# Performance work log

Hardware: AMD Instinct MI355X
Metric: run time of the kernel (lower is better)

The kernel has to match this reference:

```python
import jax, jax.numpy as jnp
import numpy as np

N = 8192
D = 256
DENSITY = 0.02  # ~164 neighbors per node


def setup_inputs() -> dict:
    key = jax.random.key(0)
    k1, k2, k3, k4 = jax.random.split(key, 4)
    inputs = jax.random.normal(k1, (N, D), dtype=jnp.float32)
    vals = jax.random.uniform(k2, (N, N), dtype=jnp.float32, minval=0.1, maxval=1.0)
    mask = jax.random.uniform(k3, (N, N), dtype=jnp.float32) < DENSITY
    adj = jnp.where(mask, vals, 0.0)
    H_v = 0.1 * jax.random.normal(k4, (D, 1), dtype=jnp.float32)
    return {"inputs": inputs, "adj": adj, "H_v": H_v}


def reference(inputs, adj, H_v):
    # scores[j] = inputs[j] . H_v  -> sparse values v_ij = adj_ij * scores[j]
    scores = jnp.squeeze(inputs @ H_v, -1)            # [N]
    mask = adj != 0.0                                  # nonzero pattern of SparseTensor
    logits = adj * scores[None, :]                     # [N, N]
    neg = jnp.asarray(jnp.finfo(logits.dtype).min, logits.dtype)
    logits = jnp.where(mask, logits, neg)
    # sparse softmax: normalize only over nonzero entries per row
    m = jnp.max(logits, axis=1, keepdims=True)
    e = jnp.where(mask, jnp.exp(logits - m), 0.0)
    s = jnp.sum(e, axis=1, keepdims=True)
    weights = e / jnp.where(s > 0, s, 1.0)             # empty rows -> all-zero weights
    # sparse_tensor_dense_matmul(weights, inputs)
    return weights @ inputs                            # [N, D]
```

## Files before the change

### kernel.cpp

```cpp
#include <hip/hip_runtime.h>

#define NN 8192
#define DD 256
#define CAP 1024

typedef float v4f __attribute__((ext_vector_type(4)));
typedef unsigned short u16x4 __attribute__((ext_vector_type(4)));

__device__ __forceinline__ unsigned short f2bf_rne(float x) {
    unsigned u = __float_as_uint(x);
    u += 0x7fffu + ((u >> 16) & 1u);
    return (unsigned short)(u >> 16);
}

__device__ __forceinline__ float4 bf4_to_f4(u16x4 u) {
    float4 r;
    r.x = __uint_as_float((unsigned)u.x << 16);
    r.y = __uint_as_float((unsigned)u.y << 16);
    r.z = __uint_as_float((unsigned)u.z << 16);
    r.w = __uint_as_float((unsigned)u.w << 16);
    return r;
}

__global__ __launch_bounds__(256) void prep_kernel(const float* __restrict__ inputs,
                                                   const float* __restrict__ Hv,
                                                   float* __restrict__ scores,
                                                   unsigned short* __restrict__ ib) {
    int wave = threadIdx.x >> 6;
    int lane = threadIdx.x & 63;
    int row  = blockIdx.x * 4 + wave;
    float4 v = ((const float4*)(inputs + (size_t)row * DD))[lane];
    u16x4 u;
    u.x = f2bf_rne(v.x); u.y = f2bf_rne(v.y); u.z = f2bf_rne(v.z); u.w = f2bf_rne(v.w);
    ((u16x4*)(ib + (size_t)row * DD))[lane] = u;
    float4 h = ((const float4*)Hv)[lane];
    float s = v.x * h.x + v.y * h.y + v.z * h.z + v.w * h.w;
    #pragma unroll
    for (int off = 32; off > 0; off >>= 1) s += __shfl_down(s, off, 64);
    if (lane == 0) scores[row] = s;
}

template <bool BF16>
__device__ __forceinline__ float4 load_row4(const float* __restrict__ inputs,
                                            const unsigned short* __restrict__ ib,
                                            int j, int lane4) {
    if (BF16) return bf4_to_f4(*(const u16x4*)(ib + (size_t)j * DD + lane4));
    else      return *(const float4*)(inputs + (size_t)j * DD + lane4);
}

template <bool BF16>
__device__ __forceinline__ void gather_accum(const float2* __restrict__ s_je,
                                             int kbeg, int kend,
                                             const float* __restrict__ inputs,
                                             const unsigned short* __restrict__ ib,
                                             int lane, int lane4,
                                             float4& acc, float& ssum) {
    for (int base = kbeg; base < kend; base += 64) {
        int nb = kend - base; nb = nb > 64 ? 64 : nb;
        float2 je = s_je[base + (lane < nb ? lane : 0)];
        int jl = __float_as_int(je.x);
        int el = __float_as_int(je.y);
        int m = 0;
        for (; m + 8 <= nb; m += 8) {
            int js[8]; float es[8]; float4 f[8];
            #pragma unroll
            for (int u = 0; u < 8; ++u) {
                js[u] = __builtin_amdgcn_readlane(jl, m + u);
                es[u] = __uint_as_float(__builtin_amdgcn_readlane(el, m + u));
            }
            #pragma unroll
            for (int u = 0; u < 8; ++u) f[u] = load_row4<BF16>(inputs, ib, js[u], lane4);
            #pragma unroll
            for (int u = 0; u < 8; ++u) {
                acc.x += es[u] * f[u].x; acc.y += es[u] * f[u].y;
                acc.z += es[u] * f[u].z; acc.w += es[u] * f[u].w;
                ssum  += es[u];
            }
        }
        for (; m < nb; ++m) {
            int   j = __builtin_amdgcn_readlane(jl, m);
            float e = __uint_as_float(__builtin_amdgcn_readlane(el, m));
            float4 f = load_row4<BF16>(inputs, ib, j, lane4);
            acc.x += e * f.x; acc.y += e * f.y; acc.z += e * f.z; acc.w += e * f.w;
            ssum += e;
        }
    }
}

template <bool BF16>
__global__ __launch_bounds__(256) void attn_kernel(const float* __restrict__ adj,
                                                   const float* __restrict__ inputs,
                                                   const unsigned short* __restrict__ ib,
                                                   const float* __restrict__ scores,
                                                   float* __restrict__ out) {
    __shared__ float2 s_je[CAP];
    __shared__ int   s_wsum[4];
    __shared__ float s_ssum[4];
    __shared__ int   s_cnt;
    __shared__ float s_red[4 * DD];

    const int row   = blockIdx.x;
    const int tid   = threadIdx.x;
    const int lane  = tid & 63;
    const int wave  = tid >> 6;
    const int lane4 = lane * 4;

    const v4f* arow4 = (const v4f*)(adj + (size_t)row * NN);
    v4f a[8];
#pragma unroll
    for (int c = 0; c < 8; ++c) a[c] = __builtin_nontemporal_load(&arow4[c * 256 + tid]);

    int nz = 0;
#pragma unroll
    for (int c = 0; c < 8; ++c)
        nz += (a[c].x != 0.f) + (a[c].y != 0.f) + (a[c].z != 0.f) + (a[c].w != 0.f);

    int pre = nz;
#pragma unroll
    for (int off = 1; off < 64; off <<= 1) {
        int t = __shfl_up(pre, off, 64);
        if (lane >= off) pre += t;
    }
    if (lane == 63) s_wsum[wave] = pre;
    __syncthreads();
    int base = 0, total = 0;
#pragma unroll
    for (int w = 0; w < 4; ++w) {
        int t = s_wsum[w];
        if (w < wave) base += t;
        total += t;
    }

    float4 acc = make_float4(0.f, 0.f, 0.f, 0.f);
    float ssum = 0.f;

    if (total <= CAP) {
        int off = base + pre - nz;
#pragma unroll
        for (int c = 0; c < 8; ++c) {
            int j0 = c * 1024 + tid * 4;
            float v;
            v = a[c].x; if (v != 0.f) { s_je[off++] = make_float2(__int_as_float(j0 + 0), __expf(v * scores[j0 + 0])); }
            v = a[c].y; if (v != 0.f) { s_je[off++] = make_float2(__int_as_float(j0 + 1), __expf(v * scores[j0 + 1])); }
            v = a[c].z; if (v != 0.f) { s_je[off++] = make_float2(__int_as_float(j0 + 2), __expf(v * scores[j0 + 2])); }
            v = a[c].w; if (v != 0.f) { s_je[off++] = make_float2(__int_as_float(j0 + 3), __expf(v * scores[j0 + 3])); }
        }
        __syncthreads();
        gather_accum<BF16>(s_je, wave * total / 4, (wave + 1) * total / 4,
                           inputs, ib, lane, lane4, acc, ssum);
    } else {
        for (int c = 0; c < 8; ++c) {
            if (tid == 0) s_cnt = 0;
            __syncthreads();
            int j0 = c * 1024 + tid * 4;
            float v;
            v = a[c].x; if (v != 0.f) { int k = atomicAdd(&s_cnt, 1); s_je[k] = make_float2(__int_as_float(j0 + 0), __expf(v * scores[j0 + 0])); }
            v = a[c].y; if (v != 0.f) { int k = atomicAdd(&s_cnt, 1); s_je[k] = make_float2(__int_as_float(j0 + 1), __expf(v * scores[j0 + 1])); }
            v = a[c].z; if (v != 0.f) { int k = atomicAdd(&s_cnt, 1); s_je[k] = make_float2(__int_as_float(j0 + 2), __expf(v * scores[j0 + 2])); }
            v = a[c].w; if (v != 0.f) { int k = atomicAdd(&s_cnt, 1); s_je[k] = make_float2(__int_as_float(j0 + 3), __expf(v * scores[j0 + 3])); }
            __syncthreads();
            int tc = s_cnt;
            gather_accum<BF16>(s_je, wave * tc / 4, (wave + 1) * tc / 4,
                               inputs, ib, lane, lane4, acc, ssum);
            __syncthreads();
        }
    }

    if (lane == 0) s_ssum[wave] = ssum;
    *(float4*)&s_red[wave * DD + lane4] = acc;
    __syncthreads();
    float tot = s_ssum[0] + s_ssum[1] + s_ssum[2] + s_ssum[3];
    float r = s_red[0 * DD + tid] + s_red[1 * DD + tid] + s_red[2 * DD + tid] + s_red[3 * DD + tid];
    out[(size_t)row * DD + tid] = (tot > 0.f) ? r / tot : 0.f;
}

extern "C" void kernel_launch(void* const* d_in, const int* in_sizes, int n_in,
                              void* d_out, int out_size, void* d_ws, size_t ws_size,
                              hipStream_t stream) {
    const float* inputs = (const float*)d_in[0];
    const float* adj    = (const float*)d_in[1];
    const float* Hv     = (const float*)d_in[2];
    float* out = (float*)d_out;

    float* scores = (float*)d_ws;
    unsigned short* ib = (unsigned short*)((char*)d_ws + NN * sizeof(float));

    const size_t need = NN * sizeof(float) + (size_t)NN * DD * sizeof(unsigned short);

    if (ws_size >= need) {
        prep_kernel<<<NN / 4, 256, 0, stream>>>(inputs, Hv, scores, ib);
        attn_kernel<true><<<NN, 256, 0, stream>>>(adj, inputs, ib, scores, out);
    } else {
        prep_kernel<<<NN / 4, 256, 0, stream>>>(inputs, Hv, scores, ib );
        attn_kernel<false><<<NN, 256, 0, stream>>>(adj, inputs, (const unsigned short*)nullptr, scores, out);
    }
}
```

Before: 405.3 us.

## Split fused attention into CSR build kernel and separate gather kernel

The single fused kernel, which both scanned the dense adjacency row and gathered neighbour features, is split in two. A build kernel compacts each row's nonzeros into a global CSR buffer holding column index and exp weight. A separate gather kernel then reads that compact list and accumulates bf16 feature rows. The aim is to separate the streaming-bandwidth phase from the latency-bound gather phase so each can run at its own occupancy. In exchange it adds a global write and re-read of the CSR buffer and one more kernel launch.

```diff
diff --git a/kernel.cpp b/kernel.cpp
--- a/kernel.cpp
+++ b/kernel.cpp
@@ -2,7 +2,7 @@
 
 #define NN 8192
 #define DD 256
-#define CAP 1024
+#define RCAP 512
 
 typedef float v4f __attribute__((ext_vector_type(4)));
 typedef unsigned short u16x4 __attribute__((ext_vector_type(4)));
@@ -22,6 +22,7 @@
     return r;
 }
 
+template <bool WRITE_IB>
 __global__ __launch_bounds__(256) void prep_kernel(const float* __restrict__ inputs,
                                                    const float* __restrict__ Hv,
                                                    float* __restrict__ scores,
@@ -30,9 +31,11 @@
     int lane = threadIdx.x & 63;
     int row  = blockIdx.x * 4 + wave;
     float4 v = ((const float4*)(inputs + (size_t)row * DD))[lane];
-    u16x4 u;
-    u.x = f2bf_rne(v.x); u.y = f2bf_rne(v.y); u.z = f2bf_rne(v.z); u.w = f2bf_rne(v.w);
-    ((u16x4*)(ib + (size_t)row * DD))[lane] = u;
+    if (WRITE_IB) {
+        u16x4 u;
+        u.x = f2bf_rne(v.x); u.y = f2bf_rne(v.y); u.z = f2bf_rne(v.z); u.w = f2bf_rne(v.w);
+        ((u16x4*)(ib + (size_t)row * DD))[lane] = u;
+    }
     float4 h = ((const float4*)Hv)[lane];
     float s = v.x * h.x + v.y * h.y + v.z * h.z + v.w * h.w;
     #pragma unroll
@@ -40,24 +43,74 @@
     if (lane == 0) scores[row] = s;
 }
 
-template <bool BF16>
-__device__ __forceinline__ float4 load_row4(const float* __restrict__ inputs,
-                                            const unsigned short* __restrict__ ib,
-                                            int j, int lane4) {
-    if (BF16) return bf4_to_f4(*(const u16x4*)(ib + (size_t)j * DD + lane4));
-    else      return *(const float4*)(inputs + (size_t)j * DD + lane4);
-}
-
-template <bool BF16>
-__device__ __forceinline__ void gather_accum(const float2* __restrict__ s_je,
+__global__ __launch_bounds__(256) void build_kernel(const float* __restrict__ adj,
+                                                    const float* __restrict__ scores,
+                                                    float2* __restrict__ csr,
+                                                    int* __restrict__ cnt) {
+    __shared__ float2 s_ja[RCAP];
+    __shared__ int s_wsum[4];
+
+    const int row  = blockIdx.x;
+    const int tid  = threadIdx.x;
+    const int lane = tid & 63;
+    const int wave = tid >> 6;
+
+    const v4f* arow4 = (const v4f*)(adj + (size_t)row * NN);
+    v4f a[8];
+#pragma unroll
+    for (int c = 0; c < 8; ++c) a[c] = arow4[c * 256 + tid];
+
+    int nz = 0;
+#pragma unroll
+    for (int c = 0; c < 8; ++c)
+        nz += (a[c].x != 0.f) + (a[c].y != 0.f) + (a[c].z != 0.f) + (a[c].w != 0.f);
+
+    int pre = nz;
+#pragma unroll
+    for (int off = 1; off < 64; off <<= 1) {
+        int t = __shfl_up(pre, off, 64);
+        if (lane >= off) pre += t;
+    }
+    if (lane == 63) s_wsum[wave] = pre;
+    __syncthreads();
+    int base = 0, total = 0;
+#pragma unroll
+    for (int w = 0; w < 4; ++w) {
+        int t = s_wsum[w];
+        if (w < wave) base += t;
+        total += t;
+    }
+
+    int off = base + pre - nz;
+#pragma unroll
+    for (int c = 0; c < 8; ++c) {
+        int j0 = c * 1024 + tid * 4;
+        float v;
+        v = a[c].x; if (v != 0.f) { if (off < RCAP) s_ja[off] = make_float2(__int_as_float(j0 + 0), v); off++; }
+        v = a[c].y; if (v != 0.f) { if (off < RCAP) s_ja[off] = make_float2(__int_as_float(j0 + 1), v); off++; }
+        v = a[c].z; if (v != 0.f) { if (off < RCAP) s_ja[off] = make_float2(__int_as_float(j0 + 2), v); off++; }
+        v = a[c].w; if (v != 0.f) { if (off < RCAP) s_ja[off] = make_float2(__int_as_float(j0 + 3), v); off++; }
+    }
+    __syncthreads();
+
+    int lim = total <= RCAP ? total : RCAP;
+    for (int k = tid; k < lim; k += 256) {
+        float2 ja = s_ja[k];
+        int j = __float_as_int(ja.x);
+        float e = __expf(ja.y * scores[j]);
+        csr[(size_t)row * RCAP + k] = make_float2(ja.x, e);
+    }
+    if (tid == 0) cnt[row] = total;
+}
+
+__device__ __forceinline__ void gather_range(const float2* __restrict__ entries,
                                              int kbeg, int kend,
-                                             const float* __restrict__ inputs,
                                              const unsigned short* __restrict__ ib,
                                              int lane, int lane4,
                                              float4& acc, float& ssum) {
-    for (int base = kbeg; base < kend; base += 64) {
-        int nb = kend - base; nb = nb > 64 ? 64 : nb;
-        float2 je = s_je[base + (lane < nb ? lane : 0)];
+    for (int b = kbeg; b < kend; b += 64) {
+        int nb = kend - b; nb = nb > 64 ? 64 : nb;
+        float2 je = entries[b + (lane < nb ? lane : 0)];
         int jl = __float_as_int(je.x);
         int el = __float_as_int(je.y);
         int m = 0;
@@ -69,7 +122,8 @@
                 es[u] = __uint_as_float(__builtin_amdgcn_readlane(el, m + u));
             }
             #pragma unroll
-            for (int u = 0; u < 8; ++u) f[u] = load_row4<BF16>(inputs, ib, js[u], lane4);
+            for (int u = 0; u < 8; ++u)
+                f[u] = bf4_to_f4(*(const u16x4*)(ib + (size_t)js[u] * DD + lane4));
             #pragma unroll
             for (int u = 0; u < 8; ++u) {
                 acc.x += es[u] * f[u].x; acc.y += es[u] * f[u].y;
@@ -80,24 +134,23 @@
         for (; m < nb; ++m) {
             int   j = __builtin_amdgcn_readlane(jl, m);
             float e = __uint_as_float(__builtin_amdgcn_readlane(el, m));
-            float4 f = load_row4<BF16>(inputs, ib, j, lane4);
+            float4 f = bf4_to_f4(*(const u16x4*)(ib + (size_t)j * DD + lane4));
             acc.x += e * f.x; acc.y += e * f.y; acc.z += e * f.z; acc.w += e * f.w;
             ssum += e;
         }
     }
 }
 
-template <bool BF16>
-__global__ __launch_bounds__(256) void attn_kernel(const float* __restrict__ adj,
-                                                   const float* __restrict__ inputs,
-                                                   const unsigned short* __restrict__ ib,
-                                                   const float* __restrict__ scores,
-                                                   float* __restrict__ out) {
-    __shared__ float2 s_je[CAP];
-    __shared__ int   s_wsum[4];
-    __shared__ float s_ssum[4];
-    __shared__ int   s_cnt;
-    __shared__ float s_red[4 * DD];
+__global__ __launch_bounds__(256) void gather_kernel(const float2* __restrict__ csr,
+                                                     const int* __restrict__ cnt,
+                                                     const unsigned short* __restrict__ ib,
+                                                     const float* __restrict__ adj,
+                                                     const float* __restrict__ scores,
+                                                     float* __restrict__ out) {
+    __shared__ float  s_red[4 * DD];
+    __shared__ float  s_ssum[4];
+    __shared__ float2 s_je[1024];
+    __shared__ int    s_cnt;
 
     const int row   = blockIdx.x;
     const int tid   = threadIdx.x;
@@ -105,63 +158,30 @@
     const int wave  = tid >> 6;
     const int lane4 = lane * 4;
 
-    const v4f* arow4 = (const v4f*)(adj + (size_t)row * NN);
-    v4f a[8];
-#pragma unroll
-    for (int c = 0; c < 8; ++c) a[c] = __builtin_nontemporal_load(&arow4[c * 256 + tid]);
-
-    int nz = 0;
-#pragma unroll
-    for (int c = 0; c < 8; ++c)
-        nz += (a[c].x != 0.f) + (a[c].y != 0.f) + (a[c].z != 0.f) + (a[c].w != 0.f);
-
-    int pre = nz;
-#pragma unroll
-    for (int off = 1; off < 64; off <<= 1) {
-        int t = __shfl_up(pre, off, 64);
-        if (lane >= off) pre += t;
-    }
-    if (lane == 63) s_wsum[wave] = pre;
-    __syncthreads();
-    int base = 0, total = 0;
-#pragma unroll
-    for (int w = 0; w < 4; ++w) {
-        int t = s_wsum[w];
-        if (w < wave) base += t;
-        total += t;
-    }
-
+    int total = cnt[row];
     float4 acc = make_float4(0.f, 0.f, 0.f, 0.f);
     float ssum = 0.f;
 
-    if (total <= CAP) {
-        int off = base + pre - nz;
-#pragma unroll
-        for (int c = 0; c < 8; ++c) {
-            int j0 = c * 1024 + tid * 4;
-            float v;
-            v = a[c].x; if (v != 0.f) { s_je[off++] = make_float2(__int_as_float(j0 + 0), __expf(v * scores[j0 + 0])); }
-            v = a[c].y; if (v != 0.f) { s_je[off++] = make_float2(__int_as_float(j0 + 1), __expf(v * scores[j0 + 1])); }
-            v = a[c].z; if (v != 0.f) { s_je[off++] = make_float2(__int_as_float(j0 + 2), __expf(v * scores[j0 + 2])); }
-            v = a[c].w; if (v != 0.f) { s_je[off++] = make_float2(__int_as_float(j0 + 3), __expf(v * scores[j0 + 3])); }
-        }
-        __syncthreads();
-        gather_accum<BF16>(s_je, wave * total / 4, (wave + 1) * total / 4,
-                           inputs, ib, lane, lane4, acc, ssum);
+    if (total <= RCAP) {
+        const float2* rowp = csr + (size_t)row * RCAP;
+        gather_range(rowp, wave * total / 4, (wave + 1) * total / 4,
+                     ib, lane, lane4, acc, ssum);
     } else {
+        const float* arow = adj + (size_t)row * NN;
         for (int c = 0; c < 8; ++c) {
             if (tid == 0) s_cnt = 0;
             __syncthreads();
+            float4 a = ((const float4*)(arow + c * 1024))[tid];
             int j0 = c * 1024 + tid * 4;
             float v;
-            v = a[c].x; if (v != 0.f) { int k = atomicAdd(&s_cnt, 1); s_je[k] = make_float2(__int_as_float(j0 + 0), __expf(v * scores[j0 + 0])); }
-            v = a[c].y; if (v != 0.f) { int k = atomicAdd(&s_cnt, 1); s_je[k] = make_float2(__int_as_float(j0 + 1), __expf(v * scores[j0 + 1])); }
-            v = a[c].z; if (v != 0.f) { int k = atomicAdd(&s_cnt, 1); s_je[k] = make_float2(__int_as_float(j0 + 2), __expf(v * scores[j0 + 2])); }
-            v = a[c].w; if (v != 0.f) { int k = atomicAdd(&s_cnt, 1); s_je[k] = make_float2(__int_as_float(j0 + 3), __expf(v * scores[j0 + 3])); }
+            v = a.x; if (v != 0.f) { int k = atomicAdd(&s_cnt, 1); s_je[k] = make_float2(__int_as_float(j0 + 0), __expf(v * scores[j0 + 0])); }
+            v = a.y; if (v != 0.f) { int k = atomicAdd(&s_cnt, 1); s_je[k] = make_float2(__int_as_float(j0 + 1), __expf(v * scores[j0 + 1])); }
+            v = a.z; if (v != 0.f) { int k = atomicAdd(&s_cnt, 1); s_je[k] = make_float2(__int_as_float(j0 + 2), __expf(v * scores[j0 + 2])); }
+            v = a.w; if (v != 0.f) { int k = atomicAdd(&s_cnt, 1); s_je[k] = make_float2(__int_as_float(j0 + 3), __expf(v * scores[j0 + 3])); }
             __syncthreads();
             int tc = s_cnt;
-            gather_accum<BF16>(s_je, wave * tc / 4, (wave + 1) * tc / 4,
-                               inputs, ib, lane, lane4, acc, ssum);
+            gather_range(s_je, wave * tc / 4, (wave + 1) * tc / 4,
+                         ib, lane, lane4, acc, ssum);
             __syncthreads();
         }
     }
@@ -172,6 +192,38 @@
     float tot = s_ssum[0] + s_ssum[1] + s_ssum[2] + s_ssum[3];
     float r = s_red[0 * DD + tid] + s_red[1 * DD + tid] + s_red[2 * DD + tid] + s_red[3 * DD + tid];
     out[(size_t)row * DD + tid] = (tot > 0.f) ? r / tot : 0.f;
+}
+
+__global__ __launch_bounds__(256) void attn_fallback(const float* __restrict__ adj,
+                                                     const float* __restrict__ inputs,
+                                                     const float* __restrict__ scores,
+                                                     float* __restrict__ out) {
+    __shared__ int   s_j[1024];
+    __shared__ float s_e[1024];
+    __shared__ int   s_cnt;
+    const int row = blockIdx.x;
+    const int tid = threadIdx.x;
+    const float* arow = adj + (size_t)row * NN;
+    float acc = 0.f, ssum = 0.f;
+    for (int base = 0; base < NN; base += 1024) {
+        if (tid == 0) s_cnt = 0;
+        __syncthreads();
+        float4 a = ((const float4*)(arow + base))[tid];
+        int j0 = base + tid * 4;
+        if (a.x != 0.f) { int k = atomicAdd(&s_cnt, 1); s_j[k] = j0 + 0; s_e[k] = __expf(a.x * scores[j0 + 0]); }
+        if (a.y != 0.f) { int k = atomicAdd(&s_cnt, 1); s_j[k] = j0 + 1; s_e[k] = __expf(a.y * scores[j0 + 1]); }
+        if (a.z != 0.f) { int k = atomicAdd(&s_cnt, 1); s_j[k] = j0 + 2; s_e[k] = __expf(a.z * scores[j0 + 2]); }
+        if (a.w != 0.f) { int k = atomicAdd(&s_cnt, 1); s_j[k] = j0 + 3; s_e[k] = __expf(a.w * scores[j0 + 3]); }
+        __syncthreads();
+        int c = s_cnt;
+        for (int k = 0; k < c; ++k) {
+            float e = s_e[k];
+            acc  += e * inputs[(size_t)s_j[k] * DD + tid];
+            ssum += e;
+        }
+        __syncthreads();
+    }
+    out[(size_t)row * DD + tid] = (ssum > 0.f) ? acc / ssum : 0.f;
 }
 
 extern "C" void kernel_launch(void* const* d_in, const int* in_sizes, int n_in,
@@ -182,16 +234,20 @@
     const float* Hv     = (const float*)d_in[2];
     float* out = (float*)d_out;
 
-    float* scores = (float*)d_ws;
-    unsigned short* ib = (unsigned short*)((char*)d_ws + NN * sizeof(float));
-
-    const size_t need = NN * sizeof(float) + (size_t)NN * DD * sizeof(unsigned short);
+    char* ws = (char*)d_ws;
+    float*          scores = (float*)ws;
+    unsigned short* ib     = (unsigned short*)(ws + 32768);
+    int*            cnt    = (int*)(ws + 32768 + (size_t)NN * DD * 2);
+    float2*         csr    = (float2*)(ws + 65536 + (size_t)NN * DD * 2);
+
+    const size_t need = 65536 + (size_t)NN * DD * 2 + (size_t)NN * RCAP * sizeof(float2);
 
     if (ws_size >= need) {
-        prep_kernel<<<NN / 4, 256, 0, stream>>>(inputs, Hv, scores, ib);
-        attn_kernel<true><<<NN, 256, 0, stream>>>(adj, inputs, ib, scores, out);
+        prep_kernel<true><<<NN / 4, 256, 0, stream>>>(inputs, Hv, scores, ib);
+        build_kernel<<<NN, 256, 0, stream>>>(adj, scores, csr, cnt);
+        gather_kernel<<<NN, 256, 0, stream>>>(csr, cnt, ib, adj, scores, out);
     } else {
-        prep_kernel<<<NN / 4, 256, 0, stream>>>(inputs, Hv, scores, ib );
-        attn_kernel<false><<<NN, 256, 0, stream>>>(adj, inputs, (const unsigned short*)nullptr, scores, out);
-    }
-}
+        prep_kernel<false><<<NN / 4, 256, 0, stream>>>(inputs, Hv, scores, nullptr);
+        attn_fallback<<<NN, 256, 0, stream>>>(adj, inputs, scores, out);
+    }
+}
```

After: 410.1 us. No clear change (+1.2%).
